# Kernel tuning notes

Measured on AMD Instinct MI355X. Metric: run time of the kernel, lower is better.

Reference implementation:

```python
import jax, jax.numpy as jnp
import numpy as np

BATCH = 32
NUM_ANCHORS = 3
NUM_CLASSES = 80
GRID = 52
INP_DIM = 416


def setup_inputs() -> dict:
    key = jax.random.key(0)
    k1, _ = jax.random.split(key)
    prediction = jax.random.normal(
        k1, (BATCH, NUM_ANCHORS * (5 + NUM_CLASSES), GRID, GRID), dtype=jnp.float32)
    anchors = jnp.array([[10.0, 13.0], [16.0, 30.0], [33.0, 23.0]], dtype=jnp.float32)
    return {"prediction": prediction, "anchors": anchors,
            "inp_dim": INP_DIM, "num_classes": NUM_CLASSES}


def reference(prediction, anchors, inp_dim, num_classes):
    # YOLOv3 detection-head decode (targets=None inference path).
    B = prediction.shape[0]
    G = prediction.shape[2]
    stride = inp_dim // G
    A = anchors.shape[0]
    attrs = 5 + num_classes

    # [B, A, attrs, G, G] -> [B, A, G, G, attrs]  (grid dims are (gj, gi))
    p = prediction.reshape(B, A, attrs, G, G).transpose(0, 1, 3, 4, 2)

    anc = anchors / stride  # anchors in grid units, [A, 2]

    xy = jax.nn.sigmoid(p[..., 0:2])          # sigmoid(tx), sigmoid(ty)
    conf = jax.nn.sigmoid(p[..., 4:5])
    cls = jax.nn.sigmoid(p[..., 5:])

    g = jnp.arange(G, dtype=p.dtype)
    x_off = g.reshape(1, 1, 1, G)   # varies along gi (last spatial axis)
    y_off = g.reshape(1, 1, G, 1)   # varies along gj

    # Torch code detaches x/y/w/h before decoding into box coords.
    bx = jax.lax.stop_gradient(xy[..., 0]) + x_off
    by = jax.lax.stop_gradient(xy[..., 1]) + y_off
    bw = jnp.exp(jax.lax.stop_gradient(p[..., 2])) * anc[:, 0].reshape(1, A, 1, 1)
    bh = jnp.exp(jax.lax.stop_gradient(p[..., 3])) * anc[:, 1].reshape(1, A, 1, 1)

    coords = jnp.stack([bx, by, bw, bh], axis=-1) * stride  # back to pixel units
    pred = jnp.concatenate([coords, conf, cls], axis=-1)    # [B, A, G, G, attrs]
    # permute(0,2,3,1,4).view(B, G*G*A, attrs)
    pred = pred.transpose(0, 2, 3, 1, 4).reshape(B, G * G * A, attrs)
    return pred
```

## Files before the change

kernel.cpp:

```cpp
#include <hip/hip_runtime.h>
#include <math.h>


#define GG 52
#define NROWS 255
#define PLANE 2704
#define NGRP 5408
#define L2E 1.442695040889f

typedef float f32x4 __attribute__((ext_vector_type(4)));

__device__ __forceinline__ float fast_sigmoid(float x) {
    return __builtin_amdgcn_rcpf(1.0f + __builtin_amdgcn_exp2f(-L2E * x));
}

__global__ __launch_bounds__(256, 8)
void detect_decode_kernel(const float* __restrict__ in,
                          const float* __restrict__ anchors,
                          float* __restrict__ out) {
    __shared__ float tile[16 * NROWS];

    const int B    = blockIdx.x;
    const int g    = (B & 7) * (NGRP / 8) + (B >> 3);
    const int b    = g / 169;
    const int s0   = (g - b * 169) * 16;
    const int gj0  = s0 / GG;
    const int rem0 = s0 - gj0 * GG;
    const int t    = threadIdx.x;

    const float* __restrict__ src = in + (size_t)b * NROWS * PLANE + s0;

    const float a0x = anchors[0], a0y = anchors[1];
    const float a1x = anchors[2], a1y = anchors[3];
    const float a2x = anchors[4], a2y = anchors[5];

    #pragma unroll
    for (int it = 0; it < 4; ++it) {
        int idx = t + it * 256;
        if (idx > 1019) idx = 1019;
        const int c = idx >> 2;
        const int q = idx & 3;

        const f32x4 v = *reinterpret_cast<const f32x4*>(
            src + (size_t)c * PLANE + 4 * q);

        f32x4 r;
        r.x = fast_sigmoid(v.x);
        r.y = fast_sigmoid(v.y);
        r.z = fast_sigmoid(v.z);
        r.w = fast_sigmoid(v.w);

        const bool sp0 = c < 4;
        const bool sp1 = (unsigned)(c - 85)  < 4u;
        const bool sp2 = (unsigned)(c - 170) < 4u;
        if (__builtin_expect(sp0 | sp1 | sp2, 0)) {
            const int attr = sp0 ? c : (sp1 ? c - 85 : c - 170);
            const float ancx = sp0 ? a0x : (sp1 ? a1x : a2x);
            const float ancy = sp0 ? a0y : (sp1 ? a1y : a2y);
            const float anc  = (attr == 2) ? ancx : ancy;
            #pragma unroll
            for (int k = 0; k < 4; ++k) {
                const int rem = rem0 + 4 * q + k;
                const int wv  = (rem >= GG) ? 1 : 0;
                const int gi  = rem - (wv ? GG : 0);
                const int gj  = gj0 + wv;
                const float x  = v[k];
                const float sg = r[k];
                float rr;
                if (attr == 0)      rr = (sg + (float)gi) * 8.0f;
                else if (attr == 1) rr = (sg + (float)gj) * 8.0f;
                else                rr = __builtin_amdgcn_exp2f(L2E * x) * anc;
                r[k] = rr;
            }
        }

        const int e = q * 4 * NROWS + c;
        tile[e            ] = r.x;
        tile[e +     NROWS] = r.y;
        tile[e + 2 * NROWS] = r.z;
        tile[e + 3 * NROWS] = r.w;
    }

    __syncthreads();

    float* __restrict__ dst = out + ((size_t)b * PLANE + s0) * NROWS;

    const int i0 = t;
    const int i1 = t + 256;
    const int i2 = t + 512;
    const int i3 = (t + 768 < 1020) ? t + 768 : 1019;

    const f32x4 u0 = *reinterpret_cast<const f32x4*>(&tile[4 * i0]);
    const f32x4 u1 = *reinterpret_cast<const f32x4*>(&tile[4 * i1]);
    const f32x4 u2 = *reinterpret_cast<const f32x4*>(&tile[4 * i2]);
    const f32x4 u3 = *reinterpret_cast<const f32x4*>(&tile[4 * i3]);

    *reinterpret_cast<f32x4*>(dst + 4 * i0) = u0;
    *reinterpret_cast<f32x4*>(dst + 4 * i1) = u1;
    *reinterpret_cast<f32x4*>(dst + 4 * i2) = u2;
    *reinterpret_cast<f32x4*>(dst + 4 * i3) = u3;
}

extern "C" void kernel_launch(void* const* d_in, const int* in_sizes, int n_in,
                              void* d_out, int out_size, void* d_ws, size_t ws_size,
                              hipStream_t stream) {
    const float* pred    = (const float*)d_in[0];
    const float* anchors = (const float*)d_in[1];
    float* out = (float*)d_out;

    detect_decode_kernel<<<NGRP, 256, 0, stream>>>(pred, anchors, out);
}
```

Baseline: 31.53 us.

## Process two tiles per block and overlap second load with first store

Halves the grid so each block handles two 16-position tiles, mapped per XCD as g0 and g0+338. The global loads for the second tile are issued before the first tile's shared-memory readback and global store, so their latency can overlap. The cost is more registers per thread, an extra barrier, and half as many blocks in flight.

```diff
diff --git a/kernel.cpp b/kernel.cpp
--- a/kernel.cpp
+++ b/kernel.cpp
@@ -5,7 +5,6 @@
 #define GG 52
 #define NROWS 255
 #define PLANE 2704
-#define NGRP 5408
 #define L2E 1.442695040889f
 
 typedef float f32x4 __attribute__((ext_vector_type(4)));
@@ -21,84 +20,114 @@
     __shared__ float tile[16 * NROWS];
 
     const int B    = blockIdx.x;
-    const int g    = (B & 7) * (NGRP / 8) + (B >> 3);
-    const int b    = g / 169;
-    const int s0   = (g - b * 169) * 16;
-    const int gj0  = s0 / GG;
-    const int rem0 = s0 - gj0 * GG;
+    const int xcd  = B & 7;
+    const int slot = B >> 3;
+    const int g0   = xcd * 676 + slot;
     const int t    = threadIdx.x;
-
-    const float* __restrict__ src = in + (size_t)b * NROWS * PLANE + s0;
-
-    const float a0x = anchors[0], a0y = anchors[1];
-    const float a1x = anchors[2], a1y = anchors[3];
-    const float a2x = anchors[4], a2y = anchors[5];
-
-    #pragma unroll
-    for (int it = 0; it < 4; ++it) {
-        int idx = t + it * 256;
-        if (idx > 1019) idx = 1019;
-        const int c = idx >> 2;
-        const int q = idx & 3;
-
-        const f32x4 v = *reinterpret_cast<const f32x4*>(
-            src + (size_t)c * PLANE + 4 * q);
-
-        f32x4 r;
-        r.x = fast_sigmoid(v.x);
-        r.y = fast_sigmoid(v.y);
-        r.z = fast_sigmoid(v.z);
-        r.w = fast_sigmoid(v.w);
-
-        const bool sp0 = c < 4;
-        const bool sp1 = (unsigned)(c - 85)  < 4u;
-        const bool sp2 = (unsigned)(c - 170) < 4u;
-        if (__builtin_expect(sp0 | sp1 | sp2, 0)) {
-            const int attr = sp0 ? c : (sp1 ? c - 85 : c - 170);
-            const float ancx = sp0 ? a0x : (sp1 ? a1x : a2x);
-            const float ancy = sp0 ? a0y : (sp1 ? a1y : a2y);
-            const float anc  = (attr == 2) ? ancx : ancy;
-            #pragma unroll
-            for (int k = 0; k < 4; ++k) {
-                const int rem = rem0 + 4 * q + k;
-                const int wv  = (rem >= GG) ? 1 : 0;
-                const int gi  = rem - (wv ? GG : 0);
-                const int gj  = gj0 + wv;
-                const float x  = v[k];
-                const float sg = r[k];
-                float rr;
-                if (attr == 0)      rr = (sg + (float)gi) * 8.0f;
-                else if (attr == 1) rr = (sg + (float)gj) * 8.0f;
-                else                rr = __builtin_amdgcn_exp2f(L2E * x) * anc;
-                r[k] = rr;
-            }
-        }
-
-        const int e = q * 4 * NROWS + c;
-        tile[e            ] = r.x;
-        tile[e +     NROWS] = r.y;
-        tile[e + 2 * NROWS] = r.z;
-        tile[e + 3 * NROWS] = r.w;
-    }
-
-    __syncthreads();
-
-    float* __restrict__ dst = out + ((size_t)b * PLANE + s0) * NROWS;
 
     const int i0 = t;
     const int i1 = t + 256;
     const int i2 = t + 512;
     const int i3 = (t + 768 < 1020) ? t + 768 : 1019;
 
-    const f32x4 u0 = *reinterpret_cast<const f32x4*>(&tile[4 * i0]);
-    const f32x4 u1 = *reinterpret_cast<const f32x4*>(&tile[4 * i1]);
-    const f32x4 u2 = *reinterpret_cast<const f32x4*>(&tile[4 * i2]);
-    const f32x4 u3 = *reinterpret_cast<const f32x4*>(&tile[4 * i3]);
+    const float a0x = anchors[0], a0y = anchors[1];
+    const float a1x = anchors[2], a1y = anchors[3];
+    const float a2x = anchors[4], a2y = anchors[5];
 
-    *reinterpret_cast<f32x4*>(dst + 4 * i0) = u0;
-    *reinterpret_cast<f32x4*>(dst + 4 * i1) = u1;
-    *reinterpret_cast<f32x4*>(dst + 4 * i2) = u2;
-    *reinterpret_cast<f32x4*>(dst + 4 * i3) = u3;
+    auto geom = [&](int g, const float*& src, float*& dst, int& gj0, int& rem0) {
+        const int b  = g / 169;
+        const int s0 = (g - b * 169) * 16;
+        src  = in  + (size_t)b * NROWS * PLANE + s0;
+        dst  = out + ((size_t)b * PLANE + s0) * NROWS;
+        gj0  = s0 / GG;
+        rem0 = s0 - gj0 * GG;
+    };
+
+    auto load4 = [&](const float* __restrict__ src, f32x4* v) {
+        v[0] = *reinterpret_cast<const f32x4*>(src + (size_t)(i0 >> 2) * PLANE + (i0 & 3) * 4);
+        v[1] = *reinterpret_cast<const f32x4*>(src + (size_t)(i1 >> 2) * PLANE + (i1 & 3) * 4);
+        v[2] = *reinterpret_cast<const f32x4*>(src + (size_t)(i2 >> 2) * PLANE + (i2 & 3) * 4);
+        v[3] = *reinterpret_cast<const f32x4*>(src + (size_t)(i3 >> 2) * PLANE + (i3 & 3) * 4);
+    };
+
+    auto decode_scatter = [&](const f32x4* v, int gj0, int rem0) {
+        #pragma unroll
+        for (int it = 0; it < 4; ++it) {
+            const int idx = (it == 0) ? i0 : (it == 1) ? i1 : (it == 2) ? i2 : i3;
+            const int c = idx >> 2;
+            const int q = idx & 3;
+            const f32x4 u = v[it];
+
+            f32x4 r;
+            r.x = fast_sigmoid(u.x);
+            r.y = fast_sigmoid(u.y);
+            r.z = fast_sigmoid(u.z);
+            r.w = fast_sigmoid(u.w);
+
+            const bool sp0 = c < 4;
+            const bool sp1 = (unsigned)(c - 85)  < 4u;
+            const bool sp2 = (unsigned)(c - 170) < 4u;
+            if (__builtin_expect(sp0 | sp1 | sp2, 0)) {
+                const int attr = sp0 ? c : (sp1 ? c - 85 : c - 170);
+                const float ancx = sp0 ? a0x : (sp1 ? a1x : a2x);
+                const float ancy = sp0 ? a0y : (sp1 ? a1y : a2y);
+                const float anc  = (attr == 2) ? ancx : ancy;
+                #pragma unroll
+                for (int k = 0; k < 4; ++k) {
+                    const int rem = rem0 + 4 * q + k;
+                    const int wv  = (rem >= GG) ? 1 : 0;
+                    const int gi  = rem - (wv ? GG : 0);
+                    const int gj  = gj0 + wv;
+                    const float x  = u[k];
+                    const float sg = r[k];
+                    float rr;
+                    if (attr == 0)      rr = (sg + (float)gi) * 8.0f;
+                    else if (attr == 1) rr = (sg + (float)gj) * 8.0f;
+                    else                rr = __builtin_amdgcn_exp2f(L2E * x) * anc;
+                    r[k] = rr;
+                }
+            }
+
+            const int e = q * 4 * NROWS + c;
+            tile[e            ] = r.x;
+            tile[e +     NROWS] = r.y;
+            tile[e + 2 * NROWS] = r.z;
+            tile[e + 3 * NROWS] = r.w;
+        }
+    };
+
+    auto read_store = [&](float* __restrict__ dst) {
+        const f32x4 u0 = *reinterpret_cast<const f32x4*>(&tile[4 * i0]);
+        const f32x4 u1 = *reinterpret_cast<const f32x4*>(&tile[4 * i1]);
+        const f32x4 u2 = *reinterpret_cast<const f32x4*>(&tile[4 * i2]);
+        const f32x4 u3 = *reinterpret_cast<const f32x4*>(&tile[4 * i3]);
+        *reinterpret_cast<f32x4*>(dst + 4 * i0) = u0;
+        *reinterpret_cast<f32x4*>(dst + 4 * i1) = u1;
+        *reinterpret_cast<f32x4*>(dst + 4 * i2) = u2;
+        *reinterpret_cast<f32x4*>(dst + 4 * i3) = u3;
+    };
+
+    const float* src0; float* dst0; int gj00, rem00;
+    const float* src1; float* dst1; int gj01, rem01;
+    geom(g0,       src0, dst0, gj00, rem00);
+    geom(g0 + 338, src1, dst1, gj01, rem01);
+
+    f32x4 v[4];
+
+    load4(src0, v);
+    decode_scatter(v, gj00, rem00);
+    __syncthreads();
+
+    f32x4 w[4];
+    load4(src1, w);
+
+    read_store(dst0);
+    __syncthreads();
+
+    decode_scatter(w, gj01, rem01);
+    __syncthreads();
+
+    read_store(dst1);
 }
 
 extern "C" void kernel_launch(void* const* d_in, const int* in_sizes, int n_in,
@@ -108,5 +137,5 @@
     const float* anchors = (const float*)d_in[1];
     float* out = (float*)d_out;
 
-    detect_decode_kernel<<<NGRP, 256, 0, stream>>>(pred, anchors, out);
+    detect_decode_kernel<<<2704, 256, 0, stream>>>(pred, anchors, out);
 }
```

New measurement: 49.52 us. 1.57x slower.

## Process two tiles per block with prefetched second-tile loads

Applied to the files above, without the earlier changes.

Halves the grid so each block handles two 16-cell groups. The global loads for the second group are issued before the first group's tile is written out, overlapping load latency with the store phase. This reduces block count and launch/scheduling overhead, in exchange for higher register pressure and an extra barrier. The XCD-aware group mapping is adjusted so each XCD still covers contiguous groups.

```diff
diff --git a/kernel.cpp b/kernel.cpp
--- a/kernel.cpp
+++ b/kernel.cpp
@@ -5,13 +5,59 @@
 #define GG 52
 #define NROWS 255
 #define PLANE 2704
-#define NGRP 5408
 #define L2E 1.442695040889f
 
 typedef float f32x4 __attribute__((ext_vector_type(4)));
 
 __device__ __forceinline__ float fast_sigmoid(float x) {
     return __builtin_amdgcn_rcpf(1.0f + __builtin_amdgcn_exp2f(-L2E * x));
+}
+
+__device__ __forceinline__ f32x4 decode4(f32x4 u, int idx, int gj0, int rem0,
+                                         float a0x, float a0y, float a1x,
+                                         float a1y, float a2x, float a2y) {
+    const int c = idx >> 2;
+    const int q = idx & 3;
+
+    f32x4 r;
+    r.x = fast_sigmoid(u.x);
+    r.y = fast_sigmoid(u.y);
+    r.z = fast_sigmoid(u.z);
+    r.w = fast_sigmoid(u.w);
+
+    const bool sp0 = c < 4;
+    const bool sp1 = (unsigned)(c - 85)  < 4u;
+    const bool sp2 = (unsigned)(c - 170) < 4u;
+    if (__builtin_expect(sp0 | sp1 | sp2, 0)) {
+        const int attr = sp0 ? c : (sp1 ? c - 85 : c - 170);
+        const float ancx = sp0 ? a0x : (sp1 ? a1x : a2x);
+        const float ancy = sp0 ? a0y : (sp1 ? a1y : a2y);
+        const float anc  = (attr == 2) ? ancx : ancy;
+        #pragma unroll
+        for (int k = 0; k < 4; ++k) {
+            const int rem = rem0 + 4 * q + k;
+            const int wv  = (rem >= GG) ? 1 : 0;
+            const int gi  = rem - (wv ? GG : 0);
+            const int gj  = gj0 + wv;
+            const float x  = u[k];
+            const float sg = r[k];
+            float rr;
+            if (attr == 0)      rr = (sg + (float)gi) * 8.0f;
+            else if (attr == 1) rr = (sg + (float)gj) * 8.0f;
+            else                rr = __builtin_amdgcn_exp2f(L2E * x) * anc;
+            r[k] = rr;
+        }
+    }
+    return r;
+}
+
+__device__ __forceinline__ void scatter4(float* __restrict__ tile, int idx,
+                                         f32x4 r) {
+    const int e = (idx & 3) * 4 * NROWS + (idx >> 2);
+    tile[e            ] = r.x;
+    tile[e +     NROWS] = r.y;
+    tile[e + 2 * NROWS] = r.z;
+    tile[e + 3 * NROWS] = r.w;
 }
 
 __global__ __launch_bounds__(256, 8)
@@ -21,84 +67,82 @@
     __shared__ float tile[16 * NROWS];
 
     const int B    = blockIdx.x;
-    const int g    = (B & 7) * (NGRP / 8) + (B >> 3);
-    const int b    = g / 169;
-    const int s0   = (g - b * 169) * 16;
-    const int gj0  = s0 / GG;
-    const int rem0 = s0 - gj0 * GG;
+    const int xcd  = B & 7;
+    const int slot = B >> 3;
+    const int g0   = xcd * 676 + slot;
+    const int g1   = g0 + 338;
     const int t    = threadIdx.x;
-
-    const float* __restrict__ src = in + (size_t)b * NROWS * PLANE + s0;
-
-    const float a0x = anchors[0], a0y = anchors[1];
-    const float a1x = anchors[2], a1y = anchors[3];
-    const float a2x = anchors[4], a2y = anchors[5];
-
-    #pragma unroll
-    for (int it = 0; it < 4; ++it) {
-        int idx = t + it * 256;
-        if (idx > 1019) idx = 1019;
-        const int c = idx >> 2;
-        const int q = idx & 3;
-
-        const f32x4 v = *reinterpret_cast<const f32x4*>(
-            src + (size_t)c * PLANE + 4 * q);
-
-        f32x4 r;
-        r.x = fast_sigmoid(v.x);
-        r.y = fast_sigmoid(v.y);
-        r.z = fast_sigmoid(v.z);
-        r.w = fast_sigmoid(v.w);
-
-        const bool sp0 = c < 4;
-        const bool sp1 = (unsigned)(c - 85)  < 4u;
-        const bool sp2 = (unsigned)(c - 170) < 4u;
-        if (__builtin_expect(sp0 | sp1 | sp2, 0)) {
-            const int attr = sp0 ? c : (sp1 ? c - 85 : c - 170);
-            const float ancx = sp0 ? a0x : (sp1 ? a1x : a2x);
-            const float ancy = sp0 ? a0y : (sp1 ? a1y : a2y);
-            const float anc  = (attr == 2) ? ancx : ancy;
-            #pragma unroll
-            for (int k = 0; k < 4; ++k) {
-                const int rem = rem0 + 4 * q + k;
-                const int wv  = (rem >= GG) ? 1 : 0;
-                const int gi  = rem - (wv ? GG : 0);
-                const int gj  = gj0 + wv;
-                const float x  = v[k];
-                const float sg = r[k];
-                float rr;
-                if (attr == 0)      rr = (sg + (float)gi) * 8.0f;
-                else if (attr == 1) rr = (sg + (float)gj) * 8.0f;
-                else                rr = __builtin_amdgcn_exp2f(L2E * x) * anc;
-                r[k] = rr;
-            }
-        }
-
-        const int e = q * 4 * NROWS + c;
-        tile[e            ] = r.x;
-        tile[e +     NROWS] = r.y;
-        tile[e + 2 * NROWS] = r.z;
-        tile[e + 3 * NROWS] = r.w;
-    }
-
-    __syncthreads();
-
-    float* __restrict__ dst = out + ((size_t)b * PLANE + s0) * NROWS;
 
     const int i0 = t;
     const int i1 = t + 256;
     const int i2 = t + 512;
     const int i3 = (t + 768 < 1020) ? t + 768 : 1019;
 
-    const f32x4 u0 = *reinterpret_cast<const f32x4*>(&tile[4 * i0]);
-    const f32x4 u1 = *reinterpret_cast<const f32x4*>(&tile[4 * i1]);
-    const f32x4 u2 = *reinterpret_cast<const f32x4*>(&tile[4 * i2]);
-    const f32x4 u3 = *reinterpret_cast<const f32x4*>(&tile[4 * i3]);
+    const float a0x = anchors[0], a0y = anchors[1];
+    const float a1x = anchors[2], a1y = anchors[3];
+    const float a2x = anchors[4], a2y = anchors[5];
 
-    *reinterpret_cast<f32x4*>(dst + 4 * i0) = u0;
-    *reinterpret_cast<f32x4*>(dst + 4 * i1) = u1;
-    *reinterpret_cast<f32x4*>(dst + 4 * i2) = u2;
-    *reinterpret_cast<f32x4*>(dst + 4 * i3) = u3;
+    const int b0_  = g0 / 169;
+    const int s00  = (g0 - b0_ * 169) * 16;
+    const int gj00 = s00 / GG;
+    const int rem00 = s00 - gj00 * GG;
+    const float* __restrict__ src0 = in + (size_t)b0_ * NROWS * PLANE + s00;
+    float* __restrict__ dst0 = out + ((size_t)b0_ * PLANE + s00) * NROWS;
+
+    const int b1_  = g1 / 169;
+    const int s01  = (g1 - b1_ * 169) * 16;
+    const int gj01 = s01 / GG;
+    const int rem01 = s01 - gj01 * GG;
+    const float* __restrict__ src1 = in + (size_t)b1_ * NROWS * PLANE + s01;
+    float* __restrict__ dst1 = out + ((size_t)b1_ * PLANE + s01) * NROWS;
+
+    const f32x4 va = *reinterpret_cast<const f32x4*>(src0 + (size_t)(i0 >> 2) * PLANE + (i0 & 3) * 4);
+    const f32x4 vb = *reinterpret_cast<const f32x4*>(src0 + (size_t)(i1 >> 2) * PLANE + (i1 & 3) * 4);
+    const f32x4 vc = *reinterpret_cast<const f32x4*>(src0 + (size_t)(i2 >> 2) * PLANE + (i2 & 3) * 4);
+    const f32x4 vd = *reinterpret_cast<const f32x4*>(src0 + (size_t)(i3 >> 2) * PLANE + (i3 & 3) * 4);
+
+    scatter4(tile, i0, decode4(va, i0, gj00, rem00, a0x, a0y, a1x, a1y, a2x, a2y));
+    scatter4(tile, i1, decode4(vb, i1, gj00, rem00, a0x, a0y, a1x, a1y, a2x, a2y));
+    scatter4(tile, i2, decode4(vc, i2, gj00, rem00, a0x, a0y, a1x, a1y, a2x, a2y));
+    scatter4(tile, i3, decode4(vd, i3, gj00, rem00, a0x, a0y, a1x, a1y, a2x, a2y));
+
+    __syncthreads();
+
+    const f32x4 wa = *reinterpret_cast<const f32x4*>(src1 + (size_t)(i0 >> 2) * PLANE + (i0 & 3) * 4);
+    const f32x4 wb = *reinterpret_cast<const f32x4*>(src1 + (size_t)(i1 >> 2) * PLANE + (i1 & 3) * 4);
+    const f32x4 wc = *reinterpret_cast<const f32x4*>(src1 + (size_t)(i2 >> 2) * PLANE + (i2 & 3) * 4);
+    const f32x4 wd = *reinterpret_cast<const f32x4*>(src1 + (size_t)(i3 >> 2) * PLANE + (i3 & 3) * 4);
+
+    {
+        const f32x4 u0 = *reinterpret_cast<const f32x4*>(&tile[4 * i0]);
+        const f32x4 u1 = *reinterpret_cast<const f32x4*>(&tile[4 * i1]);
+        const f32x4 u2 = *reinterpret_cast<const f32x4*>(&tile[4 * i2]);
+        const f32x4 u3 = *reinterpret_cast<const f32x4*>(&tile[4 * i3]);
+        *reinterpret_cast<f32x4*>(dst0 + 4 * i0) = u0;
+        *reinterpret_cast<f32x4*>(dst0 + 4 * i1) = u1;
+        *reinterpret_cast<f32x4*>(dst0 + 4 * i2) = u2;
+        *reinterpret_cast<f32x4*>(dst0 + 4 * i3) = u3;
+    }
+
+    __syncthreads();
+
+    scatter4(tile, i0, decode4(wa, i0, gj01, rem01, a0x, a0y, a1x, a1y, a2x, a2y));
+    scatter4(tile, i1, decode4(wb, i1, gj01, rem01, a0x, a0y, a1x, a1y, a2x, a2y));
+    scatter4(tile, i2, decode4(wc, i2, gj01, rem01, a0x, a0y, a1x, a1y, a2x, a2y));
+    scatter4(tile, i3, decode4(wd, i3, gj01, rem01, a0x, a0y, a1x, a1y, a2x, a2y));
+
+    __syncthreads();
+
+    {
+        const f32x4 u0 = *reinterpret_cast<const f32x4*>(&tile[4 * i0]);
+        const f32x4 u1 = *reinterpret_cast<const f32x4*>(&tile[4 * i1]);
+        const f32x4 u2 = *reinterpret_cast<const f32x4*>(&tile[4 * i2]);
+        const f32x4 u3 = *reinterpret_cast<const f32x4*>(&tile[4 * i3]);
+        *reinterpret_cast<f32x4*>(dst1 + 4 * i0) = u0;
+        *reinterpret_cast<f32x4*>(dst1 + 4 * i1) = u1;
+        *reinterpret_cast<f32x4*>(dst1 + 4 * i2) = u2;
+        *reinterpret_cast<f32x4*>(dst1 + 4 * i3) = u3;
+    }
 }
 
 extern "C" void kernel_launch(void* const* d_in, const int* in_sizes, int n_in,
@@ -108,5 +152,5 @@
     const float* anchors = (const float*)d_in[1];
     float* out = (float*)d_out;
 
-    detect_decode_kernel<<<NGRP, 256, 0, stream>>>(pred, anchors, out);
+    detect_decode_kernel<<<2704, 256, 0, stream>>>(pred, anchors, out);
 }
```

After: 31.80 us. Within noise of the previous version (+0.8%).
